# Performance work log

Measured on AMD Instinct MI355X. Metric: run time of the kernel, lower is better.

## Reference

```python
import jax, jax.numpy as jnp
import numpy as np

B = 16
L = 3600
LATENT = 64
D_MODEL = 128
D_INNER = 256   # expand * d_model
D_STATE = 16
D_CONV = 4
DT_RANK = 8     # ceil(d_model / 16)


def setup_inputs() -> dict:
    key = jax.random.key(0)
    ks = jax.random.split(key, 10)

    def w(k, shape, fan_in):
        return jax.random.normal(k, shape, jnp.float32) / np.float32(np.sqrt(fan_in))

    return {
        "z_sequence": jax.random.normal(ks[0], (B, L, LATENT), jnp.float32),
        # embedding Linear(latent_dim -> mamba_dim)
        "emb_w": w(ks[1], (D_MODEL, LATENT), LATENT),
        "emb_b": jnp.zeros((D_MODEL,), jnp.float32),
        # Mamba in_proj (no bias): d_model -> 2*d_inner
        "in_proj_w": w(ks[2], (2 * D_INNER, D_MODEL), D_MODEL),
        # depthwise causal conv1d (d_inner groups, kernel d_conv) + bias
        "conv_w": w(ks[3], (D_INNER, 1, D_CONV), D_CONV),
        "conv_b": jnp.zeros((D_INNER,), jnp.float32),
        # x_proj (no bias): d_inner -> dt_rank + 2*d_state
        "x_proj_w": w(ks[4], (DT_RANK + 2 * D_STATE, D_INNER), D_INNER),
        # dt_proj: dt_rank -> d_inner, bias init so softplus(b) ~ 0.01
        "dt_proj_w": w(ks[5], (D_INNER, DT_RANK), DT_RANK),
        "dt_proj_b": jnp.full((D_INNER,), np.log(np.expm1(0.01)), jnp.float32),
        # S4D-real init: A = -[1..d_state] per channel
        "A_log": jnp.log(jnp.broadcast_to(
            jnp.arange(1, D_STATE + 1, dtype=jnp.float32), (D_INNER, D_STATE))),
        "D_skip": jnp.ones((D_INNER,), jnp.float32),
        # out_proj (no bias): d_inner -> d_model
        "out_proj_w": w(ks[6], (D_MODEL, D_INNER), D_INNER),
        # LayerNorm(d_model)
        "norm_w": jnp.ones((D_MODEL,), jnp.float32),
        "norm_b": jnp.zeros((D_MODEL,), jnp.float32),
        # classifier Linear(d_model -> 1)
        "cls_w": w(ks[7], (1, D_MODEL), D_MODEL),
        "cls_b": jnp.zeros((1,), jnp.float32),
    }


def _forward(z_sequence, emb_w, emb_b, in_proj_w, conv_w, conv_b, x_proj_w,
             dt_proj_w, dt_proj_b, A_log, D_skip, out_proj_w,
             norm_w, norm_b, cls_w, cls_b):
    silu = jax.nn.silu
    # embedding: (B,L,latent) -> (B,L,d_model)
    x_emb = z_sequence @ emb_w.T + emb_b
    # Mamba in_proj -> x, z  each (B,L,d_inner)
    xz = x_emb @ in_proj_w.T
    x, z = jnp.split(xz, 2, axis=-1)
    # causal depthwise conv over time
    x_ncl = x.transpose(0, 2, 1)  # (B, d_inner, L)
    x_conv = jax.lax.conv_general_dilated(
        x_ncl, conv_w, window_strides=(1,), padding=[(D_CONV - 1, 0)],
        feature_group_count=D_INNER, dimension_numbers=("NCH", "OIH", "NCH"))
    x = silu(x_conv.transpose(0, 2, 1) + conv_b)  # (B,L,d_inner)
    # input-dependent SSM params
    x_dbl = x @ x_proj_w.T  # (B,L,dt_rank+2*d_state)
    dt_in, B_ssm, C_ssm = jnp.split(x_dbl, [DT_RANK, DT_RANK + D_STATE], axis=-1)
    dt = jax.nn.softplus(dt_in @ dt_proj_w.T + dt_proj_b)  # (B,L,d_inner)
    A = -jnp.exp(A_log)  # (d_inner, d_state)

    def step(h, inp):
        x_t, dt_t, B_t, C_t = inp  # (B,d_inner),(B,d_inner),(B,d_state),(B,d_state)
        h = jnp.exp(dt_t[:, :, None] * A) * h + (dt_t * x_t)[:, :, None] * B_t[:, None, :]
        y = jnp.einsum("bds,bs->bd", h, C_t)
        return h, y

    h0 = jnp.zeros((x.shape[0], D_INNER, D_STATE), x.dtype)
    xs = (x.transpose(1, 0, 2), dt.transpose(1, 0, 2),
          B_ssm.transpose(1, 0, 2), C_ssm.transpose(1, 0, 2))
    _, ys = jax.lax.scan(step, h0, xs)  # ys: (L,B,d_inner)
    y = ys.transpose(1, 0, 2) + x * D_skip
    y = y * silu(z)
    out = y @ out_proj_w.T  # (B,L,d_model)
    # take last timestep, LayerNorm, classify
    x_last = out[:, -1, :]
    mu = x_last.mean(-1, keepdims=True)
    var = ((x_last - mu) ** 2).mean(-1, keepdims=True)
    xn = (x_last - mu) / jnp.sqrt(var + 1e-5) * norm_w + norm_b
    logit = xn @ cls_w.T + cls_b  # (B,1)
    return logit.squeeze(-1)      # (B,)


def reference(z_sequence, emb_w, emb_b, in_proj_w, conv_w, conv_b, x_proj_w,
              dt_proj_w, dt_proj_b, A_log, D_skip, out_proj_w,
              norm_w, norm_b, cls_w, cls_b):
    return _forward(z_sequence, emb_w, emb_b, in_proj_w, conv_w, conv_b,
                    x_proj_w, dt_proj_w, dt_proj_b, A_log, D_skip,
                    out_proj_w, norm_w, norm_b, cls_w, cls_b)
```

## Files before the change

kernel.cpp:

```cpp
#include <hip/hip_runtime.h>
#include <hip/hip_bf16.h>
#include <math.h>

#define B_  16
#define L_  3600
#define LAT 64
#define DM  128
#define DI  256
#define DS  16
#define DR  8

#define TT  45
#define NT  80
#define NC  80
#define TC  45
#define THR (-20.0f)

typedef __bf16 v8bf __attribute__((ext_vector_type(8)));
typedef float  v4f  __attribute__((ext_vector_type(4)));
typedef unsigned short v8us __attribute__((ext_vector_type(8)));

#define MFMA16(A, Bf, C) __builtin_amdgcn_mfma_f32_16x16x32_bf16((A), (Bf), (C), 0, 0, 0)

__device__ __forceinline__ float siluf(float v) {
    return v * __builtin_amdgcn_rcpf(1.0f + __expf(-v));
}
__device__ __forceinline__ float softplusf(float v) {
    float r = __logf(1.0f + __expf(v));
    return (v > 15.0f) ? v : r;
}
__device__ __forceinline__ float bf2f(unsigned short u) {
    unsigned int x = ((unsigned int)u) << 16;
    return __builtin_bit_cast(float, x);
}
__device__ __forceinline__ unsigned short f2bf(float f) {
    __hip_bfloat16 h = __float2bfloat16(f);
    return __builtin_bit_cast(unsigned short, h);
}

__global__ __launch_bounds__(64) void k0_combine(
    const float* __restrict__ in_proj_w, const float* __restrict__ emb_w,
    const float* __restrict__ emb_b, const float* __restrict__ x_proj_w,
    float* __restrict__ W1, float* __restrict__ b1,
    unsigned short* __restrict__ W1h, unsigned short* __restrict__ W1l,
    unsigned short* __restrict__ xwh, unsigned short* __restrict__ xwl)
{
    int blk = blockIdx.x, k = threadIdx.x;
    if (blk < DI) {
        int d = blk;
        const float* row = in_proj_w + (size_t)d * DM;
        float acc = 0.f;
        for (int m = 0; m < DM; ++m) acc += row[m] * emb_w[m * LAT + k];
        W1[d * LAT + k] = acc;
        unsigned short h = f2bf(acc);
        W1h[d * LAT + k] = h;
        W1l[d * LAT + k] = f2bf(acc - bf2f(h));
        if (k == 0) {
            float ab = 0.f;
            for (int m = 0; m < DM; ++m) ab += row[m] * emb_b[m];
            b1[d] = ab;
        }
    } else {
        int j = blk - DI;
        int sw = (j & 7) << 3;
        #pragma unroll
        for (int q = 0; q < 4; ++q) {
            int c = k * 4 + q;
            float v = x_proj_w[(size_t)j * DI + c];
            unsigned short h = f2bf(v);
            int idx = j * 256 + (c ^ sw);
            xwh[idx] = h;
            xwl[idx] = f2bf(v - bf2f(h));
        }
    }
}

__global__ __launch_bounds__(256, 2) void k1_front(
    const float* __restrict__ z, const float* __restrict__ conv_w,
    const float* __restrict__ conv_b, const float* __restrict__ dt_proj_w,
    const float* __restrict__ dt_proj_b,
    const unsigned short* __restrict__ W1h, const unsigned short* __restrict__ W1l,
    const unsigned short* __restrict__ xwh, const unsigned short* __restrict__ xwl,
    const float* __restrict__ b1,
    float* __restrict__ Bssm, float* __restrict__ Dcs,
    __hip_bfloat16* __restrict__ x_bf, __hip_bfloat16* __restrict__ dt_bf,
    float* __restrict__ hlast)
{
    __shared__ float xpre[48 * 258];
    __shared__ unsigned short uB[12288];
    __shared__ float dtl[TT][8];

    int b = blockIdx.y, tile = blockIdx.x;
    int t0 = tile * TT;
    int t0m3 = t0 - 3;
    int tid = threadIdx.x;
    int lane = tid & 63, wid = tid >> 6;
    int l15 = lane & 15, l4 = lane >> 4;

    if (tile == 0) {
        float4 z4 = make_float4(0.f, 0.f, 0.f, 0.f);
        float4* hl4 = (float4*)(hlast + (size_t)b * (DS * DI));
        #pragma unroll
        for (int i = 0; i < 4; ++i) hl4[tid + i * 256] = z4;
    }

    float4 cw = *(const float4*)(conv_w + tid * 4);
    float cb = conv_b[tid];
    float bias = b1[tid];
    float4 dwA = *(const float4*)(dt_proj_w + (size_t)tid * DR);
    float4 dwB = *(const float4*)(dt_proj_w + (size_t)tid * DR + 4);
    float dbias = dt_proj_b[tid];

    v8bf wh[4][2], wl[4][2];
    {
        int d0w = wid * 64;
        #pragma unroll
        for (int nt = 0; nt < 4; ++nt) {
            int dr = d0w + nt * 16 + l15;
            #pragma unroll
            for (int kb = 0; kb < 2; ++kb) {
                int k0 = kb * 32 + l4 * 8;
                wh[nt][kb] = __builtin_bit_cast(v8bf, *(const v8us*)(W1h + (size_t)dr * LAT + k0));
                wl[nt][kb] = __builtin_bit_cast(v8bf, *(const v8us*)(W1l + (size_t)dr * LAT + k0));
            }
        }
    }

    {
        const float* zb = z + (size_t)b * L_ * LAT;
        for (int i = tid; i < 48 * 8; i += 256) {
            int r = i >> 3, s = i & 7;
            int tg = t0m3 + r;
            float f[8];
            if (tg >= 0) {
                float4 u = *(const float4*)(zb + (size_t)tg * LAT + s * 8);
                float4 v = *(const float4*)(zb + (size_t)tg * LAT + s * 8 + 4);
                f[0]=u.x; f[1]=u.y; f[2]=u.z; f[3]=u.w; f[4]=v.x; f[5]=v.y; f[6]=v.z; f[7]=v.w;
            } else {
                #pragma unroll
                for (int q = 0; q < 8; ++q) f[q] = 0.f;
            }
            v8us hh, ll;
            #pragma unroll
            for (int q = 0; q < 8; ++q) {
                unsigned short h = f2bf(f[q]);
                hh[q] = h;
                ll[q] = f2bf(f[q] - bf2f(h));
            }
            int idx = r * 64 + ((s * 8) ^ ((r & 7) << 3));
            *(v8us*)&uB[idx] = hh;
            *(v8us*)&uB[3072 + idx] = ll;
        }
    }
    __syncthreads();

    {
        int d0w = wid * 64;
        #pragma unroll
        for (int mt = 0; mt < 3; ++mt) {
            int r = mt * 16 + l15;
            int sw = (r & 7) << 3;
            int kb0 = l4 * 8;
            v8bf ah0 = __builtin_bit_cast(v8bf, *(const v8us*)&uB[r * 64 + (kb0 ^ sw)]);
            v8bf ah1 = __builtin_bit_cast(v8bf, *(const v8us*)&uB[r * 64 + ((32 + kb0) ^ sw)]);
            v8bf al0 = __builtin_bit_cast(v8bf, *(const v8us*)&uB[3072 + r * 64 + (kb0 ^ sw)]);
            v8bf al1 = __builtin_bit_cast(v8bf, *(const v8us*)&uB[3072 + r * 64 + ((32 + kb0) ^ sw)]);
            int rr = mt * 16 + l4 * 4;
            #pragma unroll
            for (int nt = 0; nt < 4; ++nt) {
                v4f acc = {0.f, 0.f, 0.f, 0.f};
                acc = MFMA16(ah0, wh[nt][0], acc);
                acc = MFMA16(ah1, wh[nt][1], acc);
                acc = MFMA16(ah0, wl[nt][0], acc);
                acc = MFMA16(ah1, wl[nt][1], acc);
                acc = MFMA16(al0, wh[nt][0], acc);
                acc = MFMA16(al1, wh[nt][1], acc);
                int cc = d0w + nt * 16 + l15;
                xpre[(rr + 0) * 258 + cc] = acc[0];
                xpre[(rr + 1) * 258 + cc] = acc[1];
                xpre[(rr + 2) * 258 + cc] = acc[2];
                xpre[(rr + 3) * 258 + cc] = acc[3];
            }
        }
    }

    v8us xwr[6];
    {
        #pragma unroll
        for (int p = 0; p < 3; ++p) {
            xwr[p]     = *(const v8us*)(xwh + tid * 24 + p * 8);
            xwr[3 + p] = *(const v8us*)(xwl + tid * 24 + p * 8);
        }
    }
    __syncthreads();

    float xr[TT];
    {
        int d = tid;
        float p0 = xpre[0 * 258 + d] + ((t0m3 + 0 >= 0) ? bias : 0.f);
        float p1 = xpre[1 * 258 + d] + ((t0m3 + 1 >= 0) ? bias : 0.f);
        float p2 = xpre[2 * 258 + d] + ((t0m3 + 2 >= 0) ? bias : 0.f);
        #pragma unroll
        for (int r = 3; r < 48; ++r) {
            float cur = xpre[r * 258 + d] + bias;
            float xc = cw.x * p0 + cw.y * p1 + cw.z * p2 + cw.w * cur + cb;
            xr[r - 3] = siluf(xc);
            p0 = p1; p1 = p2; p2 = cur;
        }
        __hip_bfloat16* xb = x_bf + ((size_t)b * L_ + t0) * DI + d;
        #pragma unroll
        for (int t = 0; t < TT; ++t)
            xb[(size_t)t * DI] = __float2bfloat16(xr[t]);
    }
    __syncthreads();

    unsigned short* xt16 = (unsigned short*)xpre;
    {
        int d = tid;
        #pragma unroll
        for (int t = 0; t < TT; ++t)
            xt16[t * 512 + (d ^ ((t & 7) << 3))] = f2bf(xr[t]);
        #pragma unroll
        for (int t = TT; t < 48; ++t)
            xt16[t * 512 + (d ^ ((t & 7) << 3))] = 0;
        #pragma unroll
        for (int p = 0; p < 3; ++p) {
            *(v8us*)&uB[tid * 24 + p * 8] = xwr[p];
            *(v8us*)&uB[6144 + tid * 24 + p * 8] = xwr[3 + p];
        }
    }
    __syncthreads();

    if (wid < 3) {
        int mt = wid;
        int rA = mt * 16 + l15;
        int swA = (rA & 7) << 3;
        int jc0 = l15;
        int jc1 = 16 + l15; if (jc1 > 23) jc1 = 23;
        v4f acc0 = {0.f, 0.f, 0.f, 0.f}, acc1 = {0.f, 0.f, 0.f, 0.f};
        #pragma unroll
        for (int kb = 0; kb < 8; ++kb) {
            int k0 = kb * 32 + l4 * 8;
            v8bf xa  = __builtin_bit_cast(v8bf, *(const v8us*)&xt16[rA * 512 + (k0 ^ swA)]);
            int s0 = k0 ^ ((jc0 & 7) << 3);
            int s1 = k0 ^ ((jc1 & 7) << 3);
            v8bf b0h = __builtin_bit_cast(v8bf, *(const v8us*)&uB[jc0 * 256 + s0]);
            v8bf b0l = __builtin_bit_cast(v8bf, *(const v8us*)&uB[6144 + jc0 * 256 + s0]);
            v8bf b1h = __builtin_bit_cast(v8bf, *(const v8us*)&uB[jc1 * 256 + s1]);
            v8bf b1l = __builtin_bit_cast(v8bf, *(const v8us*)&uB[6144 + jc1 * 256 + s1]);
            acc0 = MFMA16(xa, b0h, acc0);
            acc0 = MFMA16(xa, b0l, acc0);
            acc1 = MFMA16(xa, b1h, acc1);
            acc1 = MFMA16(xa, b1l, acc1);
        }
        int rr = mt * 16 + l4 * 4;
        #pragma unroll
        for (int reg = 0; reg < 4; ++reg) {
            int t = rr + reg;
            if (t < TT) {
                size_t tg = (size_t)b * L_ + (t0 + t);
                float v0 = acc0[reg], v1 = acc1[reg];
                if (l15 < 8) {
                    dtl[t][l15] = v0;
                    Bssm[tg * DS + 8 + l15] = v1;
                } else {
                    Bssm[tg * DS + (l15 - 8)] = v0;
                }
            }
        }
    }
    __syncthreads();

    {
        int d = tid;
        __hip_bfloat16* dout = dt_bf + ((size_t)b * L_ + t0) * DI + d;
        float S = 0.f;
        #pragma unroll 5
        for (int t = 0; t < TT; ++t) {
            float4 u = *(const float4*)&dtl[t][0];
            float4 v = *(const float4*)&dtl[t][4];
            float r = dbias + u.x*dwA.x + u.y*dwA.y + u.z*dwA.z + u.w*dwA.w
                            + v.x*dwB.x + v.y*dwB.y + v.z*dwB.z + v.w*dwB.w;
            float dt = softplusf(r);
            dout[(size_t)t * DI] = __float2bfloat16(dt);
            S += dt;
        }
        Dcs[((size_t)b * NC + tile) * DI + d] = S;
    }
}

__global__ __launch_bounds__(256) void k3a2_suffix(
    const float* __restrict__ Dcs, float* __restrict__ Rsuf)
{
    int b = blockIdx.x, d = threadIdx.x;
    float R = 0.f;
    for (int c = NC - 1; c >= 0; --c) {
        Rsuf[((size_t)b * NC + c) * DI + d] = R;
        R += Dcs[((size_t)b * NC + c) * DI + d];
    }
}

__global__ __launch_bounds__(512) void k3b_scan(
    const __hip_bfloat16* __restrict__ x_bf, const __hip_bfloat16* __restrict__ dt_bf,
    const float* __restrict__ Bssm, const float* __restrict__ A_log,
    const float* __restrict__ Rsuf, float* __restrict__ hlast)
{
    int c = blockIdx.x, dg = blockIdx.y, b = blockIdx.z;
    int tid = threadIdx.x;
    int dh = tid & 31;
    int s  = ((tid >> 6) << 1) | ((tid >> 5) & 1);
    int d  = dg * 32 + dh;

    float a = -__expf(A_log[d * DS + s]);
    float R = Rsuf[((size_t)b * NC + c) * DI + d];

    float H = 0.f;
    float S_run = R;
    if (!__all(a * R < THR)) {
        int t0 = c * TC;
        const __hip_bfloat16* xp = x_bf + ((size_t)b * L_ + t0) * DI + d;
        const __hip_bfloat16* dp = dt_bf + ((size_t)b * L_ + t0) * DI + d;
        const float* Bp = Bssm + ((size_t)b * L_ + t0) * DS + s;
        {
            float x4 = __bfloat162float(xp[(TC-1)*DI]);
            float d4 = __bfloat162float(dp[(TC-1)*DI]);
            float B4 = Bp[(TC-1)*DS];
            float e = __expf(a * S_run); H = fmaf(e * d4 * x4, B4, H); S_run += d4;
        }
        for (int j = TC - 5; j >= 0; j -= 4) {
            float x3 = __bfloat162float(xp[(j+3)*DI]);
            float x2 = __bfloat162float(xp[(j+2)*DI]);
            float x1 = __bfloat162float(xp[(j+1)*DI]);
            float x0 = __bfloat162float(xp[(j+0)*DI]);
            float d3 = __bfloat162float(dp[(j+3)*DI]);
            float d2 = __bfloat162float(dp[(j+2)*DI]);
            float d1 = __bfloat162float(dp[(j+1)*DI]);
            float d0 = __bfloat162float(dp[(j+0)*DI]);
            float B3 = Bp[(j+3)*DS];
            float B2 = Bp[(j+2)*DS];
            float B1 = Bp[(j+1)*DS];
            float B0 = Bp[(j+0)*DS];
            float e;
            e = __expf(a * S_run); H = fmaf(e * d3 * x3, B3, H); S_run += d3;
            e = __expf(a * S_run); H = fmaf(e * d2 * x2, B2, H); S_run += d2;
            e = __expf(a * S_run); H = fmaf(e * d1 * x1, B1, H); S_run += d1;
            e = __expf(a * S_run); H = fmaf(e * d0 * x0, B0, H); S_run += d0;
            if (__all(a * S_run < THR)) break;
        }
    }
    if (H != 0.f)
        atomicAdd(hlast + (((size_t)b * DS + s) * DI + d), H);
}

__global__ __launch_bounds__(256) void k4_final(
    const float* __restrict__ z, const float* __restrict__ emb_w,
    const float* __restrict__ emb_b, const float* __restrict__ in_proj_w,
    const float* __restrict__ conv_w, const float* __restrict__ conv_b,
    const float* __restrict__ x_proj_w, const float* __restrict__ D_skip,
    const float* __restrict__ out_proj_w, const float* __restrict__ norm_w,
    const float* __restrict__ norm_b, const float* __restrict__ cls_w,
    const float* __restrict__ cls_b, const float* __restrict__ W1,
    const float* __restrict__ b1, const float* __restrict__ h_last,
    float* __restrict__ out)
{
    __shared__ float zl[4][64];
    __shared__ float xlast[DI];
    __shared__ float xemb[DM];
    __shared__ float Cl[DS];
    __shared__ float ylds[DI];
    __shared__ float olds[DM];
    int b = blockIdx.x, tid = threadIdx.x;
    {
        int r = tid >> 6, k = tid & 63;
        zl[r][k] = z[((size_t)b * L_ + (L_ - 4 + r)) * LAT + k];
    }
    __syncthreads();
    {
        int d = tid;
        const float* wr = W1 + d * LAT;
        float xp[4];
        #pragma unroll
        for (int r = 0; r < 4; ++r) {
            float acc = b1[d];
            for (int k = 0; k < LAT; ++k) acc += zl[r][k] * wr[k];
            xp[r] = acc;
        }
        float4 cwv = *(const float4*)(conv_w + d * 4);
        float xc = cwv.x*xp[0] + cwv.y*xp[1] + cwv.z*xp[2] + cwv.w*xp[3] + conv_b[d];
        xlast[d] = siluf(xc);
    }
    __syncthreads();
    if (tid < DS) {
        float acc = 0.f;
        const float* wr = x_proj_w + (size_t)(DR + DS + tid) * DI;
        for (int k = 0; k < DI; ++k) acc += xlast[k] * wr[k];
        Cl[tid] = acc;
    }
    if (tid >= 64 && tid < 64 + DM) {
        int m = tid - 64;
        float acc = emb_b[m];
        const float* wr = emb_w + (size_t)m * LAT;
        for (int k = 0; k < LAT; ++k) acc += zl[3][k] * wr[k];
        xemb[m] = acc;
    }
    __syncthreads();
    {
        int d = tid;
        float hs = 0.f;
        #pragma unroll
        for (int si = 0; si < DS; ++si)
            hs += h_last[((size_t)b * DS + si) * DI + d] * Cl[si];
        float y = hs + xlast[d] * D_skip[d];
        float zbv = 0.f;
        const float* wr = in_proj_w + (size_t)(DI + d) * DM;
        for (int m = 0; m < DM; ++m) zbv += xemb[m] * wr[m];
        y *= siluf(zbv);
        ylds[d] = y;
    }
    __syncthreads();
    if (tid < DM) {
        float acc = 0.f;
        const float* wr = out_proj_w + (size_t)tid * DI;
        for (int k = 0; k < DI; ++k) acc += ylds[k] * wr[k];
        olds[tid] = acc;
    }
    __syncthreads();
    if (tid < 64) {
        float v0 = olds[tid], v1 = olds[tid + 64];
        float sum = v0 + v1;
        #pragma unroll
        for (int off = 32; off > 0; off >>= 1) sum += __shfl_down(sum, off);
        float mu = __shfl(sum, 0) * (1.0f / 128.0f);
        float dv0 = v0 - mu, dv1 = v1 - mu;
        float vs = dv0 * dv0 + dv1 * dv1;
        #pragma unroll
        for (int off = 32; off > 0; off >>= 1) vs += __shfl_down(vs, off);
        float var = __shfl(vs, 0) * (1.0f / 128.0f);
        float rstd = rsqrtf(var + 1e-5f);
        float xn0 = dv0 * rstd * norm_w[tid] + norm_b[tid];
        float xn1 = dv1 * rstd * norm_w[tid + 64] + norm_b[tid + 64];
        float lg = xn0 * cls_w[tid] + xn1 * cls_w[tid + 64];
        #pragma unroll
        for (int off = 32; off > 0; off >>= 1) lg += __shfl_down(lg, off);
        if (tid == 0) out[b] = lg + cls_b[0];
    }
}

extern "C" void kernel_launch(void* const* d_in, const int* in_sizes, int n_in,
                              void* d_out, int out_size, void* d_ws, size_t ws_size,
                              hipStream_t stream) {
    (void)in_sizes; (void)n_in; (void)out_size;
    const float* z         = (const float*)d_in[0];
    const float* emb_w     = (const float*)d_in[1];
    const float* emb_b     = (const float*)d_in[2];
    const float* in_proj_w = (const float*)d_in[3];
    const float* conv_w    = (const float*)d_in[4];
    const float* conv_b    = (const float*)d_in[5];
    const float* x_proj_w  = (const float*)d_in[6];
    const float* dt_proj_w = (const float*)d_in[7];
    const float* dt_proj_b = (const float*)d_in[8];
    const float* A_log     = (const float*)d_in[9];
    const float* D_skip    = (const float*)d_in[10];
    const float* out_proj_w= (const float*)d_in[11];
    const float* norm_w    = (const float*)d_in[12];
    const float* norm_b    = (const float*)d_in[13];
    const float* cls_w     = (const float*)d_in[14];
    const float* cls_b     = (const float*)d_in[15];
    float* out = (float*)d_out;

    float* ws    = (float*)d_ws;
    float* W1    = ws;
    float* b1    = W1 + 16384;
    float* Bssm  = b1 + 256;
    float* Dcs   = Bssm + 921600;
    float* Rsuf  = Dcs + 327680;
    float* hlast = Rsuf + 327680;
    float* fend  = hlast + 65536;
    unsigned short* W1h  = (unsigned short*)fend;
    unsigned short* W1l  = W1h + 16384;
    unsigned short* xwh  = W1l + 16384;
    unsigned short* xwl  = xwh + 6144;
    __hip_bfloat16* x_bf  = (__hip_bfloat16*)(xwl + 6144);
    __hip_bfloat16* dt_bf = x_bf + (size_t)B_ * L_ * DI;
    size_t needed = ((size_t)(16384 + 256 + 921600 + 327680 + 327680 + 65536)) * 4
                  + ((size_t)(16384 + 16384 + 6144 + 6144)) * 2
                  + (size_t)B_ * L_ * DI * 2 * 2;
    if (ws_size < needed) return;

    k0_combine <<<dim3(DI + 24),     dim3(LAT), 0, stream>>>(in_proj_w, emb_w, emb_b, x_proj_w,
                                                             W1, b1, W1h, W1l, xwh, xwl);
    k1_front   <<<dim3(NT, B_),      dim3(256), 0, stream>>>(z, conv_w, conv_b, dt_proj_w, dt_proj_b,
                                                             W1h, W1l, xwh, xwl, b1,
                                                             Bssm, Dcs, x_bf, dt_bf, hlast);
    k3a2_suffix<<<dim3(B_),          dim3(256), 0, stream>>>(Dcs, Rsuf);
    k3b_scan   <<<dim3(NC, 8, B_),   dim3(512), 0, stream>>>(x_bf, dt_bf, Bssm, A_log, Rsuf, hlast);
    k4_final   <<<dim3(B_),          dim3(256), 0, stream>>>(z, emb_w, emb_b, in_proj_w, conv_w, conv_b,
                                                             x_proj_w, D_skip, out_proj_w, norm_w, norm_b,
                                                             cls_w, cls_b, W1, b1, hlast, out);
}
```

Before: 121.6 us.

## Shrink k1_front shared memory via split GEMM and pack x/dt into one word

The front kernel's in-projection GEMM is split into two passes (rows 0-31, then 32-47) so the fp32 staging buffer and the other operands fit in a single aliased 48KB shared region. Launch bounds are raised to 3 blocks per CU. x and dt are now written as one packed 32-bit bf16 pair, so the scan kernel issues one load per timestep instead of two. The price is extra barriers and a second MFMA pass, plus a possible register-pressure squeeze from the higher occupancy target.

```diff
diff --git a/kernel.cpp b/kernel.cpp
--- a/kernel.cpp
+++ b/kernel.cpp
@@ -75,7 +75,7 @@
     }
 }
 
-__global__ __launch_bounds__(256, 2) void k1_front(
+__global__ __launch_bounds__(256, 3) void k1_front(
     const float* __restrict__ z, const float* __restrict__ conv_w,
     const float* __restrict__ conv_b, const float* __restrict__ dt_proj_w,
     const float* __restrict__ dt_proj_b,
@@ -83,12 +83,16 @@
     const unsigned short* __restrict__ xwh, const unsigned short* __restrict__ xwl,
     const float* __restrict__ b1,
     float* __restrict__ Bssm, float* __restrict__ Dcs,
-    __hip_bfloat16* __restrict__ x_bf, __hip_bfloat16* __restrict__ dt_bf,
-    float* __restrict__ hlast)
+    unsigned int* __restrict__ xd, float* __restrict__ hlast)
 {
-    __shared__ float xpre[48 * 258];
-    __shared__ unsigned short uB[12288];
+    __shared__ __align__(16) unsigned char smem[49152];
     __shared__ float dtl[TT][8];
+    float* xpre = (float*)smem;
+    unsigned short* zth = (unsigned short*)(smem + 32896);
+    unsigned short* ztl = (unsigned short*)(smem + 39040);
+    unsigned short* xt16 = (unsigned short*)smem;
+    unsigned short* xwhL = (unsigned short*)(smem + 24576);
+    unsigned short* xwlL = (unsigned short*)(smem + 36864);
 
     int b = blockIdx.y, tile = blockIdx.x;
     int t0 = tile * TT;
@@ -148,39 +152,37 @@
                 ll[q] = f2bf(f[q] - bf2f(h));
             }
             int idx = r * 64 + ((s * 8) ^ ((r & 7) << 3));
-            *(v8us*)&uB[idx] = hh;
-            *(v8us*)&uB[3072 + idx] = ll;
-        }
-    }
-    __syncthreads();
-
-    {
-        int d0w = wid * 64;
-        #pragma unroll
-        for (int mt = 0; mt < 3; ++mt) {
-            int r = mt * 16 + l15;
-            int sw = (r & 7) << 3;
-            int kb0 = l4 * 8;
-            v8bf ah0 = __builtin_bit_cast(v8bf, *(const v8us*)&uB[r * 64 + (kb0 ^ sw)]);
-            v8bf ah1 = __builtin_bit_cast(v8bf, *(const v8us*)&uB[r * 64 + ((32 + kb0) ^ sw)]);
-            v8bf al0 = __builtin_bit_cast(v8bf, *(const v8us*)&uB[3072 + r * 64 + (kb0 ^ sw)]);
-            v8bf al1 = __builtin_bit_cast(v8bf, *(const v8us*)&uB[3072 + r * 64 + ((32 + kb0) ^ sw)]);
-            int rr = mt * 16 + l4 * 4;
-            #pragma unroll
-            for (int nt = 0; nt < 4; ++nt) {
-                v4f acc = {0.f, 0.f, 0.f, 0.f};
-                acc = MFMA16(ah0, wh[nt][0], acc);
-                acc = MFMA16(ah1, wh[nt][1], acc);
-                acc = MFMA16(ah0, wl[nt][0], acc);
-                acc = MFMA16(ah1, wl[nt][1], acc);
-                acc = MFMA16(al0, wh[nt][0], acc);
-                acc = MFMA16(al1, wh[nt][1], acc);
-                int cc = d0w + nt * 16 + l15;
-                xpre[(rr + 0) * 258 + cc] = acc[0];
-                xpre[(rr + 1) * 258 + cc] = acc[1];
-                xpre[(rr + 2) * 258 + cc] = acc[2];
-                xpre[(rr + 3) * 258 + cc] = acc[3];
-            }
+            *(v8us*)&zth[idx] = hh;
+            *(v8us*)&ztl[idx] = ll;
+        }
+    }
+    __syncthreads();
+
+    int d0w = wid * 64;
+    #pragma unroll
+    for (int mt = 0; mt < 2; ++mt) {
+        int r = mt * 16 + l15;
+        int sw = (r & 7) << 3;
+        int kb0 = l4 * 8;
+        v8bf ah0 = __builtin_bit_cast(v8bf, *(const v8us*)&zth[r * 64 + (kb0 ^ sw)]);
+        v8bf ah1 = __builtin_bit_cast(v8bf, *(const v8us*)&zth[r * 64 + ((32 + kb0) ^ sw)]);
+        v8bf al0 = __builtin_bit_cast(v8bf, *(const v8us*)&ztl[r * 64 + (kb0 ^ sw)]);
+        v8bf al1 = __builtin_bit_cast(v8bf, *(const v8us*)&ztl[r * 64 + ((32 + kb0) ^ sw)]);
+        int rr = mt * 16 + l4 * 4;
+        #pragma unroll
+        for (int nt = 0; nt < 4; ++nt) {
+            v4f acc = {0.f, 0.f, 0.f, 0.f};
+            acc = MFMA16(ah0, wh[nt][0], acc);
+            acc = MFMA16(ah1, wh[nt][1], acc);
+            acc = MFMA16(ah0, wl[nt][0], acc);
+            acc = MFMA16(ah1, wl[nt][1], acc);
+            acc = MFMA16(al0, wh[nt][0], acc);
+            acc = MFMA16(al1, wh[nt][1], acc);
+            int cc = d0w + nt * 16 + l15;
+            xpre[(rr + 0) * 257 + cc] = acc[0];
+            xpre[(rr + 1) * 257 + cc] = acc[1];
+            xpre[(rr + 2) * 257 + cc] = acc[2];
+            xpre[(rr + 3) * 257 + cc] = acc[3];
         }
     }
 
@@ -195,38 +197,73 @@
     __syncthreads();
 
     float xr[TT];
+    float p0, p1, p2;
     {
         int d = tid;
-        float p0 = xpre[0 * 258 + d] + ((t0m3 + 0 >= 0) ? bias : 0.f);
-        float p1 = xpre[1 * 258 + d] + ((t0m3 + 1 >= 0) ? bias : 0.f);
-        float p2 = xpre[2 * 258 + d] + ((t0m3 + 2 >= 0) ? bias : 0.f);
-        #pragma unroll
-        for (int r = 3; r < 48; ++r) {
-            float cur = xpre[r * 258 + d] + bias;
+        p0 = xpre[0 * 257 + d] + ((t0m3 + 0 >= 0) ? bias : 0.f);
+        p1 = xpre[1 * 257 + d] + ((t0m3 + 1 >= 0) ? bias : 0.f);
+        p2 = xpre[2 * 257 + d] + ((t0m3 + 2 >= 0) ? bias : 0.f);
+        #pragma unroll
+        for (int r = 3; r < 32; ++r) {
+            float cur = xpre[r * 257 + d] + bias;
             float xc = cw.x * p0 + cw.y * p1 + cw.z * p2 + cw.w * cur + cb;
             xr[r - 3] = siluf(xc);
             p0 = p1; p1 = p2; p2 = cur;
         }
-        __hip_bfloat16* xb = x_bf + ((size_t)b * L_ + t0) * DI + d;
+    }
+    __syncthreads();
+
+    {
+        int r = 32 + l15;
+        int sw = (r & 7) << 3;
+        int kb0 = l4 * 8;
+        v8bf ah0 = __builtin_bit_cast(v8bf, *(const v8us*)&zth[r * 64 + (kb0 ^ sw)]);
+        v8bf ah1 = __builtin_bit_cast(v8bf, *(const v8us*)&zth[r * 64 + ((32 + kb0) ^ sw)]);
+        v8bf al0 = __builtin_bit_cast(v8bf, *(const v8us*)&ztl[r * 64 + (kb0 ^ sw)]);
+        v8bf al1 = __builtin_bit_cast(v8bf, *(const v8us*)&ztl[r * 64 + ((32 + kb0) ^ sw)]);
+        int rr = l4 * 4;
+        #pragma unroll
+        for (int nt = 0; nt < 4; ++nt) {
+            v4f acc = {0.f, 0.f, 0.f, 0.f};
+            acc = MFMA16(ah0, wh[nt][0], acc);
+            acc = MFMA16(ah1, wh[nt][1], acc);
+            acc = MFMA16(ah0, wl[nt][0], acc);
+            acc = MFMA16(ah1, wl[nt][1], acc);
+            acc = MFMA16(al0, wh[nt][0], acc);
+            acc = MFMA16(al1, wh[nt][1], acc);
+            int cc = d0w + nt * 16 + l15;
+            xpre[(rr + 0) * 257 + cc] = acc[0];
+            xpre[(rr + 1) * 257 + cc] = acc[1];
+            xpre[(rr + 2) * 257 + cc] = acc[2];
+            xpre[(rr + 3) * 257 + cc] = acc[3];
+        }
+    }
+    __syncthreads();
+
+    {
+        int d = tid;
+        #pragma unroll
+        for (int r = 32; r < 48; ++r) {
+            float cur = xpre[(r - 32) * 257 + d] + bias;
+            float xc = cw.x * p0 + cw.y * p1 + cw.z * p2 + cw.w * cur + cb;
+            xr[r - 3] = siluf(xc);
+            p0 = p1; p1 = p2; p2 = cur;
+        }
+    }
+    __syncthreads();
+
+    {
+        int d = tid;
         #pragma unroll
         for (int t = 0; t < TT; ++t)
-            xb[(size_t)t * DI] = __float2bfloat16(xr[t]);
-    }
-    __syncthreads();
-
-    unsigned short* xt16 = (unsigned short*)xpre;
-    {
-        int d = tid;
-        #pragma unroll
-        for (int t = 0; t < TT; ++t)
-            xt16[t * 512 + (d ^ ((t & 7) << 3))] = f2bf(xr[t]);
+            xt16[t * 256 + (d ^ ((t & 7) << 3))] = f2bf(xr[t]);
         #pragma unroll
         for (int t = TT; t < 48; ++t)
-            xt16[t * 512 + (d ^ ((t & 7) << 3))] = 0;
+            xt16[t * 256 + (d ^ ((t & 7) << 3))] = 0;
         #pragma unroll
         for (int p = 0; p < 3; ++p) {
-            *(v8us*)&uB[tid * 24 + p * 8] = xwr[p];
-            *(v8us*)&uB[6144 + tid * 24 + p * 8] = xwr[3 + p];
+            *(v8us*)&xwhL[tid * 24 + p * 8] = xwr[p];
+            *(v8us*)&xwlL[tid * 24 + p * 8] = xwr[3 + p];
         }
     }
     __syncthreads();
@@ -241,13 +278,13 @@
         #pragma unroll
         for (int kb = 0; kb < 8; ++kb) {
             int k0 = kb * 32 + l4 * 8;
-            v8bf xa  = __builtin_bit_cast(v8bf, *(const v8us*)&xt16[rA * 512 + (k0 ^ swA)]);
+            v8bf xa  = __builtin_bit_cast(v8bf, *(const v8us*)&xt16[rA * 256 + (k0 ^ swA)]);
             int s0 = k0 ^ ((jc0 & 7) << 3);
             int s1 = k0 ^ ((jc1 & 7) << 3);
-            v8bf b0h = __builtin_bit_cast(v8bf, *(const v8us*)&uB[jc0 * 256 + s0]);
-            v8bf b0l = __builtin_bit_cast(v8bf, *(const v8us*)&uB[6144 + jc0 * 256 + s0]);
-            v8bf b1h = __builtin_bit_cast(v8bf, *(const v8us*)&uB[jc1 * 256 + s1]);
-            v8bf b1l = __builtin_bit_cast(v8bf, *(const v8us*)&uB[6144 + jc1 * 256 + s1]);
+            v8bf b0h = __builtin_bit_cast(v8bf, *(const v8us*)&xwhL[jc0 * 256 + s0]);
+            v8bf b0l = __builtin_bit_cast(v8bf, *(const v8us*)&xwlL[jc0 * 256 + s0]);
+            v8bf b1h = __builtin_bit_cast(v8bf, *(const v8us*)&xwhL[jc1 * 256 + s1]);
+            v8bf b1l = __builtin_bit_cast(v8bf, *(const v8us*)&xwlL[jc1 * 256 + s1]);
             acc0 = MFMA16(xa, b0h, acc0);
             acc0 = MFMA16(xa, b0l, acc0);
             acc1 = MFMA16(xa, b1h, acc1);
@@ -273,7 +310,7 @@
 
     {
         int d = tid;
-        __hip_bfloat16* dout = dt_bf + ((size_t)b * L_ + t0) * DI + d;
+        unsigned int* xdout = xd + ((size_t)b * L_ + t0) * DI + d;
         float S = 0.f;
         #pragma unroll 5
         for (int t = 0; t < TT; ++t) {
@@ -282,7 +319,8 @@
             float r = dbias + u.x*dwA.x + u.y*dwA.y + u.z*dwA.z + u.w*dwA.w
                             + v.x*dwB.x + v.y*dwB.y + v.z*dwB.z + v.w*dwB.w;
             float dt = softplusf(r);
-            dout[(size_t)t * DI] = __float2bfloat16(dt);
+            unsigned int pack = ((unsigned int)f2bf(dt) << 16) | (unsigned int)f2bf(xr[t]);
+            xdout[(size_t)t * DI] = pack;
             S += dt;
         }
         Dcs[((size_t)b * NC + tile) * DI + d] = S;
@@ -301,7 +339,7 @@
 }
 
 __global__ __launch_bounds__(512) void k3b_scan(
-    const __hip_bfloat16* __restrict__ x_bf, const __hip_bfloat16* __restrict__ dt_bf,
+    const unsigned int* __restrict__ xd,
     const float* __restrict__ Bssm, const float* __restrict__ A_log,
     const float* __restrict__ Rsuf, float* __restrict__ hlast)
 {
@@ -318,24 +356,24 @@
     float S_run = R;
     if (!__all(a * R < THR)) {
         int t0 = c * TC;
-        const __hip_bfloat16* xp = x_bf + ((size_t)b * L_ + t0) * DI + d;
-        const __hip_bfloat16* dp = dt_bf + ((size_t)b * L_ + t0) * DI + d;
+        const unsigned int* xp = xd + ((size_t)b * L_ + t0) * DI + d;
         const float* Bp = Bssm + ((size_t)b * L_ + t0) * DS + s;
         {
-            float x4 = __bfloat162float(xp[(TC-1)*DI]);
-            float d4 = __bfloat162float(dp[(TC-1)*DI]);
+            unsigned int u4 = xp[(TC-1)*DI];
+            float x4 = bf2f((unsigned short)(u4 & 0xffff));
+            float d4 = bf2f((unsigned short)(u4 >> 16));
             float B4 = Bp[(TC-1)*DS];
             float e = __expf(a * S_run); H = fmaf(e * d4 * x4, B4, H); S_run += d4;
         }
         for (int j = TC - 5; j >= 0; j -= 4) {
-            float x3 = __bfloat162float(xp[(j+3)*DI]);
-            float x2 = __bfloat162float(xp[(j+2)*DI]);
-            float x1 = __bfloat162float(xp[(j+1)*DI]);
-            float x0 = __bfloat162float(xp[(j+0)*DI]);
-            float d3 = __bfloat162float(dp[(j+3)*DI]);
-            float d2 = __bfloat162float(dp[(j+2)*DI]);
-            float d1 = __bfloat162float(dp[(j+1)*DI]);
-            float d0 = __bfloat162float(dp[(j+0)*DI]);
+            unsigned int u3 = xp[(j+3)*DI];
+            unsigned int u2 = xp[(j+2)*DI];
+            unsigned int u1 = xp[(j+1)*DI];
+            unsigned int u0 = xp[(j+0)*DI];
+            float x3 = bf2f((unsigned short)(u3 & 0xffff)), d3 = bf2f((unsigned short)(u3 >> 16));
+            float x2 = bf2f((unsigned short)(u2 & 0xffff)), d2 = bf2f((unsigned short)(u2 >> 16));
+            float x1 = bf2f((unsigned short)(u1 & 0xffff)), d1 = bf2f((unsigned short)(u1 >> 16));
+            float x0 = bf2f((unsigned short)(u0 & 0xffff)), d0 = bf2f((unsigned short)(u0 >> 16));
             float B3 = Bp[(j+3)*DS];
             float B2 = Bp[(j+2)*DS];
             float B1 = Bp[(j+1)*DS];
@@ -480,20 +518,19 @@
     unsigned short* W1l  = W1h + 16384;
     unsigned short* xwh  = W1l + 16384;
     unsigned short* xwl  = xwh + 6144;
-    __hip_bfloat16* x_bf  = (__hip_bfloat16*)(xwl + 6144);
-    __hip_bfloat16* dt_bf = x_bf + (size_t)B_ * L_ * DI;
+    unsigned int*   xd   = (unsigned int*)(xwl + 6144);
     size_t needed = ((size_t)(16384 + 256 + 921600 + 327680 + 327680 + 65536)) * 4
                   + ((size_t)(16384 + 16384 + 6144 + 6144)) * 2
-                  + (size_t)B_ * L_ * DI * 2 * 2;
+                  + (size_t)B_ * L_ * DI * 4;
     if (ws_size < needed) return;
 
     k0_combine <<<dim3(DI + 24),     dim3(LAT), 0, stream>>>(in_proj_w, emb_w, emb_b, x_proj_w,
                                                              W1, b1, W1h, W1l, xwh, xwl);
     k1_front   <<<dim3(NT, B_),      dim3(256), 0, stream>>>(z, conv_w, conv_b, dt_proj_w, dt_proj_b,
                                                              W1h, W1l, xwh, xwl, b1,
-                                                             Bssm, Dcs, x_bf, dt_bf, hlast);
+                                                             Bssm, Dcs, xd, hlast);
     k3a2_suffix<<<dim3(B_),          dim3(256), 0, stream>>>(Dcs, Rsuf);
-    k3b_scan   <<<dim3(NC, 8, B_),   dim3(512), 0, stream>>>(x_bf, dt_bf, Bssm, A_log, Rsuf, hlast);
+    k3b_scan   <<<dim3(NC, 8, B_),   dim3(512), 0, stream>>>(xd, Bssm, A_log, Rsuf, hlast);
     k4_final   <<<dim3(B_),          dim3(256), 0, stream>>>(z, emb_w, emb_b, in_proj_w, conv_w, conv_b,
                                                              x_proj_w, D_skip, out_proj_w, norm_w, norm_b,
                                                              cls_w, cls_b, W1, b1, hlast, out);
```

New measurement: 116.1 us. 1.05x faster.
